# Kernel optimization log

Measured on AMD Instinct MI355X. Metric: run time of the kernel, lower is better.

The kernel has to match this reference:

```python
import jax, jax.numpy as jnp
import numpy as np

N, M, F, NBR = 100000, 12, 64, 64
EPS = 1e-5


def setup_inputs() -> dict:
    key = jax.random.key(0)
    ks = jax.random.split(key, 6)
    atom_in_fea = jax.random.normal(ks[0], (N, F), dtype=jnp.float32)
    nbr_fea = jax.random.normal(ks[1], (N, M, NBR), dtype=jnp.float32)
    bond_weights = jax.random.uniform(ks[2], (N, M), dtype=jnp.float32)
    nbr_fea_idx = jax.random.randint(ks[3], (N, M), 0, N)
    W = jax.random.normal(ks[4], (2 * F, 2 * F + NBR), dtype=jnp.float32) * 0.05
    b = jnp.zeros((2 * F,), dtype=jnp.float32)
    gamma1 = jnp.ones((2 * F,), dtype=jnp.float32)
    beta1 = jnp.zeros((2 * F,), dtype=jnp.float32)
    gamma2 = jnp.ones((F,), dtype=jnp.float32)
    beta2 = jnp.zeros((F,), dtype=jnp.float32)
    return dict(atom_in_fea=atom_in_fea, nbr_fea=nbr_fea, bond_weights=bond_weights,
                nbr_fea_idx=nbr_fea_idx, W=W, b=b, gamma1=gamma1, beta1=beta1,
                gamma2=gamma2, beta2=beta2)


def _batchnorm(x, gamma, beta):
    # training-mode BN over axis 0 with biased variance (torch BatchNorm1d)
    mean = x.mean(axis=0)
    var = ((x - mean) ** 2).mean(axis=0)
    return (x - mean) * jax.lax.rsqrt(var + EPS) * gamma + beta


def reference(atom_in_fea, nbr_fea, bond_weights, nbr_fea_idx, W, b,
              gamma1, beta1, gamma2, beta2):
    n, m = nbr_fea_idx.shape
    f = atom_in_fea.shape[1]
    atom_nbr_fea = atom_in_fea[nbr_fea_idx]                      # (N, M, F) gather
    self_fea = jnp.broadcast_to(atom_in_fea[:, None, :], (n, m, f))
    total = jnp.concatenate([self_fea, atom_nbr_fea, nbr_fea], axis=2)  # (N, M, 2F+NBR)
    gated = jnp.einsum('nmk,ok->nmo', total, W) + b              # (N, M, 2F)
    gated = _batchnorm(gated.reshape(-1, 2 * f), gamma1, beta1).reshape(n, m, 2 * f)
    nbr_filter = jax.nn.sigmoid(gated[..., :f]) * bond_weights[..., None]
    nbr_core = jax.nn.softplus(gated[..., f:]) * bond_weights[..., None]
    nbr_sumed = jnp.sum(nbr_filter * nbr_core, axis=1)           # (N, F)
    nbr_sumed = _batchnorm(nbr_sumed, gamma2, beta2)
    return jax.nn.softplus(atom_in_fea + nbr_sumed)
```

## Files before the change

### kernel.cpp

```cpp
#include <hip/hip_runtime.h>
#include <hip/hip_bf16.h>

typedef unsigned short ushort_t;
typedef __attribute__((ext_vector_type(8))) short bf16x8;
typedef __attribute__((ext_vector_type(4))) float f32x4;

#define NATOM 100000
#define NM    12
#define FD    64
#define KD    192
#define OD    128
#define NGRP  6250
#define ROWS1 1200000.0f
#define EPSBN 1e-5f


__device__ __forceinline__ float bf2f(ushort_t u) {
    unsigned int x = ((unsigned int)u) << 16;
    float f; __builtin_memcpy(&f, &x, 4); return f;
}
__device__ __forceinline__ ushort_t f2b(float f) {
    unsigned int x; __builtin_memcpy(&x, &f, 4);
    x += 0x7FFFu + ((x >> 16) & 1u);
    return (ushort_t)(x >> 16);
}

template<int DT>
__device__ __forceinline__ float ld1(const void* p, long i) {
    if constexpr (DT == 1) return bf2f(((const ushort_t*)p)[i]);
    else                   return ((const float*)p)[i];
}
template<int DT>
__device__ __forceinline__ void st1(void* p, long i, float v) {
    if constexpr (DT == 1) ((ushort_t*)p)[i] = f2b(v);
    else                   ((float*)p)[i] = v;
}
template<int DT>
__device__ __forceinline__ bf16x8 ld8(const void* p, long i) {
    if constexpr (DT == 1) {
        return *(const bf16x8*)((const ushort_t*)p + i);
    } else {
        const float4* f = (const float4*)((const float*)p + i);
        float4 a = f[0], b = f[1];
        bf16x8 r;
        r[0] = (short)f2b(a.x); r[1] = (short)f2b(a.y);
        r[2] = (short)f2b(a.z); r[3] = (short)f2b(a.w);
        r[4] = (short)f2b(b.x); r[5] = (short)f2b(b.y);
        r[6] = (short)f2b(b.z); r[7] = (short)f2b(b.w);
        return r;
    }
}

__global__ void k0_flag(const unsigned int* __restrict__ g1w, int* __restrict__ flag) {
    if (threadIdx.x == 0 && blockIdx.x == 0)
        *flag = (g1w[0] == 0x3F800000u) ? 0 : 1;
}

template<int DT>
__device__ __forceinline__ void stage_W(bf16x8* Wlds, const void* Wg, int tid) {
    for (int c = tid; c < 3072; c += 256) {
        int g = c >> 6, l = c & 63;
        int t = g / 6, s = g % 6;
        int row = t * 16 + (l & 15);
        int col = s * 32 + (l >> 4) * 8;
        Wlds[c] = ld8<DT>(Wg, row * KD + col);
    }
}

template<int DT>
__global__ __launch_bounds__(256) void k1_stats(
    const void* __restrict__ atomg, const void* __restrict__ nbrg,
    const int* __restrict__ idxg, const void* __restrict__ Wg,
    const int* __restrict__ flag, float* __restrict__ s1sum, float* __restrict__ s1sq)
{
    if (*flag != DT) return;
    __shared__ __align__(16) bf16x8 Wlds[3072];
    const int tid = threadIdx.x;
    const int w = tid >> 6, lane = tid & 63, la = lane & 15, q = lane >> 4;

    stage_W<DT>(Wlds, Wg, tid);
    __syncthreads();

    float sum[8], sq[8];
#pragma unroll
    for (int t = 0; t < 8; ++t) { sum[t] = 0.f; sq[t] = 0.f; }

    for (int grp = blockIdx.x; grp < NGRP; grp += gridDim.x) {
        const int n0 = grp << 4;
        const long selfo = (long)(n0 + la) * FD + q * 8;
        for (int it = 0; it < 3; ++it) {
            const int m = it * 4 + w;
            const int nb = idxg[(n0 + la) * NM + m];

            bf16x8 af[6];
            af[0] = ld8<DT>(atomg, selfo);
            af[1] = ld8<DT>(atomg, selfo + 32);
            af[2] = ld8<DT>(atomg, (long)nb * FD + q * 8);
            af[3] = ld8<DT>(atomg, (long)nb * FD + q * 8 + 32);
            af[4] = ld8<DT>(nbrg, ((long)(n0 + la) * NM + m) * FD + q * 8);
            af[5] = ld8<DT>(nbrg, ((long)(n0 + la) * NM + m) * FD + q * 8 + 32);

            f32x4 acc[8];
#pragma unroll
            for (int t = 0; t < 8; ++t) acc[t] = (f32x4){0.f, 0.f, 0.f, 0.f};
#pragma unroll
            for (int s = 0; s < 6; ++s) {
#pragma unroll
                for (int t = 0; t < 8; ++t) {
                    bf16x8 bfr = Wlds[(t * 6 + s) * 64 + lane];
                    acc[t] = __builtin_amdgcn_mfma_f32_16x16x32_bf16(af[s], bfr, acc[t], 0, 0, 0);
                }
            }
#pragma unroll
            for (int t = 0; t < 8; ++t)
#pragma unroll
                for (int r = 0; r < 4; ++r) {
                    float v = acc[t][r];
                    sum[t] += v; sq[t] += v * v;
                }
        }
    }

    const int rep = blockIdx.x & 7;
#pragma unroll
    for (int t = 0; t < 8; ++t) {
        float s = sum[t], z = sq[t];
        s += __shfl_xor(s, 16); s += __shfl_xor(s, 32);
        z += __shfl_xor(z, 16); z += __shfl_xor(z, 32);
        if (lane < 16) {
            atomicAdd(&s1sum[rep * OD + t * 16 + lane], s);
            atomicAdd(&s1sq [rep * OD + t * 16 + lane], z);
        }
    }
}

template<int DT>
__global__ __launch_bounds__(256) void k2_main(
    const void* __restrict__ atomg, const void* __restrict__ nbrg,
    const void* __restrict__ bwg, const int* __restrict__ idxg,
    const void* __restrict__ Wg,
    const void* __restrict__ g1p, const void* __restrict__ b1p,
    const float* __restrict__ s1sum, const float* __restrict__ s1sq,
    const int* __restrict__ flag,
    void* __restrict__ nsum, float* __restrict__ s2sum, float* __restrict__ s2sq)
{
    if (*flag != DT) return;
    __shared__ __align__(16) bf16x8 Wlds[3072];
    __shared__ float pred[4][16][64];
    const int tid = threadIdx.x;
    const int w = tid >> 6, lane = tid & 63, la = lane & 15, q = lane >> 4;

    stage_W<DT>(Wlds, Wg, tid);

    float scale[8], shift[8];
#pragma unroll
    for (int t = 0; t < 8; ++t) {
        int o = t * 16 + la;
        float sm = 0.f, sv = 0.f;
#pragma unroll
        for (int r = 0; r < 8; ++r) { sm += s1sum[r * OD + o]; sv += s1sq[r * OD + o]; }
        float mean = sm / ROWS1;
        float var  = sv / ROWS1 - mean * mean;
        float inv  = 1.0f / sqrtf(var + EPSBN);
        float ga   = ld1<DT>(g1p, o) * inv;
        scale[t] = ga;
        shift[t] = ld1<DT>(b1p, o) - mean * ga;
    }
    __syncthreads();

    float bsum = 0.f, bsq = 0.f;

    for (int grp = blockIdx.x; grp < NGRP; grp += gridDim.x) {
        const int n0 = grp << 4;
        const long selfo = (long)(n0 + la) * FD + q * 8;
        float psum[4][4];
#pragma unroll
        for (int t = 0; t < 4; ++t)
#pragma unroll
            for (int r = 0; r < 4; ++r) psum[t][r] = 0.f;

        for (int it = 0; it < 3; ++it) {
            const int m = it * 4 + w;
            const int nb = idxg[(n0 + la) * NM + m];

            bf16x8 af[6];
            af[0] = ld8<DT>(atomg, selfo);
            af[1] = ld8<DT>(atomg, selfo + 32);
            af[2] = ld8<DT>(atomg, (long)nb * FD + q * 8);
            af[3] = ld8<DT>(atomg, (long)nb * FD + q * 8 + 32);
            af[4] = ld8<DT>(nbrg, ((long)(n0 + la) * NM + m) * FD + q * 8);
            af[5] = ld8<DT>(nbrg, ((long)(n0 + la) * NM + m) * FD + q * 8 + 32);

            f32x4 acc[8];
#pragma unroll
            for (int t = 0; t < 8; ++t) acc[t] = (f32x4){0.f, 0.f, 0.f, 0.f};
#pragma unroll
            for (int s = 0; s < 6; ++s) {
#pragma unroll
                for (int t = 0; t < 8; ++t) {
                    bf16x8 bfr = Wlds[(t * 6 + s) * 64 + lane];
                    acc[t] = __builtin_amdgcn_mfma_f32_16x16x32_bf16(af[s], bfr, acc[t], 0, 0, 0);
                }
            }
#pragma unroll
            for (int r = 0; r < 4; ++r) {
                float bwv = ld1<DT>(bwg, (long)(n0 + q * 4 + r) * NM + m);
                float b2 = bwv * bwv;
#pragma unroll
                for (int t = 0; t < 4; ++t) {
                    float y1 = acc[t][r]     * scale[t]     + shift[t];
                    float y2 = acc[t + 4][r] * scale[t + 4] + shift[t + 4];
                    float sg = 1.0f / (1.0f + __expf(-y1));
                    float ax = fabsf(y2);
                    float sp = fmaxf(y2, 0.0f) + __logf(1.0f + __expf(-ax));
                    psum[t][r] += sg * sp * b2;
                }
            }
        }

#pragma unroll
        for (int t = 0; t < 4; ++t)
#pragma unroll
            for (int r = 0; r < 4; ++r)
                pred[w][q * 4 + r][t * 16 + la] = psum[t][r];
        __syncthreads();
        for (int e = tid; e < 1024; e += 256) {
            int a = e >> 6, c = e & 63;
            float v = pred[0][a][c] + pred[1][a][c] + pred[2][a][c] + pred[3][a][c];
            float vr;
            if constexpr (DT == 1) {
                ushort_t h = f2b(v);
                ((ushort_t*)nsum)[(long)(n0 + a) * FD + c] = h;
                vr = bf2f(h);
            } else {
                ((float*)nsum)[(long)(n0 + a) * FD + c] = v;
                vr = v;
            }
            bsum += vr; bsq += vr * vr;
        }
        __syncthreads();
    }

    const int rep = blockIdx.x & 7;
    atomicAdd(&s2sum[rep * FD + (tid & 63)], bsum);
    atomicAdd(&s2sq [rep * FD + (tid & 63)], bsq);
}

template<int DT>
__global__ __launch_bounds__(256) void k3_final(
    const void* __restrict__ atomg, void* __restrict__ nsum_out,
    const float* __restrict__ s2sum, const float* __restrict__ s2sq,
    const void* __restrict__ g2p, const void* __restrict__ b2p,
    const int* __restrict__ flag)
{
    if (*flag != DT) return;
    const int tid = blockIdx.x * 256 + threadIdx.x;
    const int c = tid & 63;
    float sm = 0.f, sv = 0.f;
#pragma unroll
    for (int r = 0; r < 8; ++r) { sm += s2sum[r * FD + c]; sv += s2sq[r * FD + c]; }
    float mean = sm / 100000.0f;
    float var  = sv / 100000.0f - mean * mean;
    float inv  = 1.0f / sqrtf(var + EPSBN);
    float ga   = ld1<DT>(g2p, c) * inv;
    float sh   = ld1<DT>(b2p, c) - mean * ga;
    float v = ld1<DT>(nsum_out, tid) * ga + sh + ld1<DT>(atomg, tid);
    float ax = fabsf(v);
    float sp = fmaxf(v, 0.0f) + __logf(1.0f + __expf(-ax));
    st1<DT>(nsum_out, tid, sp);
}

extern "C" void kernel_launch(void* const* d_in, const int* in_sizes, int n_in,
                              void* d_out, int out_size, void* d_ws, size_t ws_size,
                              hipStream_t stream) {
    const void* atomg = d_in[0];
    const void* nbrg  = d_in[1];
    const void* bwg   = d_in[2];
    const int*  idxg  = (const int*)d_in[3];
    const void* Wg    = d_in[4];
    const void* g1p   = d_in[6];
    const void* b1p   = d_in[7];
    const void* g2p   = d_in[8];
    const void* b2p   = d_in[9];

    float* wsf   = (float*)d_ws;
    float* s1sum = wsf;
    float* s1sq  = wsf + 1024;
    float* s2sum = wsf + 2048;
    float* s2sq  = wsf + 2560;
    int*   flag  = (int*)(wsf + 4000);

    hipMemsetAsync(d_ws, 0, 16384, stream);

    k0_flag<<<1, 64, 0, stream>>>((const unsigned int*)g1p, flag);

    k1_stats<0><<<768, 256, 0, stream>>>(atomg, nbrg, idxg, Wg, flag, s1sum, s1sq);
    k1_stats<1><<<768, 256, 0, stream>>>(atomg, nbrg, idxg, Wg, flag, s1sum, s1sq);

    k2_main<0><<<512, 256, 0, stream>>>(atomg, nbrg, bwg, idxg, Wg, g1p, b1p,
                                        s1sum, s1sq, flag, d_out, s2sum, s2sq);
    k2_main<1><<<512, 256, 0, stream>>>(atomg, nbrg, bwg, idxg, Wg, g1p, b1p,
                                        s1sum, s1sq, flag, d_out, s2sum, s2sq);

    k3_final<0><<<(NATOM * FD) / 256, 256, 0, stream>>>(atomg, d_out, s2sum, s2sq,
                                                        g2p, b2p, flag);
    k3_final<1><<<(NATOM * FD) / 256, 256, 0, stream>>>(atomg, d_out, s2sum, s2sq,
                                                        g2p, b2p, flag);
}
```

Baseline: 974.1 us.

## Remap k2 rows so each wave owns whole atoms; reduce via shuffles, prefetch loads

In k2, the 16 MFMA rows of each wave now hold 4 atoms × 4 neighbor slots instead of 16 atoms × 1 slot. This lets the per-atom neighbor sum be finished with cross-lane shuffles rather than an LDS buffer and two block barriers per group. Both k1 and k2 hoist the self-feature and index loads out of the neighbor loop; k1 also issues all gathers for a group before its MFMAs so the loads overlap. Launch bounds now request 3 blocks per CU and the k2 grid grows to 768, which trades register headroom for occupancy.

```diff
diff --git a/kernel.cpp b/kernel.cpp
--- a/kernel.cpp
+++ b/kernel.cpp
@@ -68,7 +68,7 @@
 }
 
 template<int DT>
-__global__ __launch_bounds__(256) void k1_stats(
+__global__ __launch_bounds__(256, 3) void k1_stats(
     const void* __restrict__ atomg, const void* __restrict__ nbrg,
     const int* __restrict__ idxg, const void* __restrict__ Wg,
     const int* __restrict__ flag, float* __restrict__ s1sum, float* __restrict__ s1sq)
@@ -88,21 +88,31 @@
     for (int grp = blockIdx.x; grp < NGRP; grp += gridDim.x) {
         const int n0 = grp << 4;
         const long selfo = (long)(n0 + la) * FD + q * 8;
+
+        const int ib = (n0 + la) * NM + w;
+        int nbv[3] = { idxg[ib], idxg[ib + 4], idxg[ib + 8] };
+
+        bf16x8 s0 = ld8<DT>(atomg, selfo);
+        bf16x8 s1 = ld8<DT>(atomg, selfo + 32);
+
+        bf16x8 a2[3], a3[3], a4[3], a5[3];
+#pragma unroll
         for (int it = 0; it < 3; ++it) {
             const int m = it * 4 + w;
-            const int nb = idxg[(n0 + la) * NM + m];
-
-            bf16x8 af[6];
-            af[0] = ld8<DT>(atomg, selfo);
-            af[1] = ld8<DT>(atomg, selfo + 32);
-            af[2] = ld8<DT>(atomg, (long)nb * FD + q * 8);
-            af[3] = ld8<DT>(atomg, (long)nb * FD + q * 8 + 32);
-            af[4] = ld8<DT>(nbrg, ((long)(n0 + la) * NM + m) * FD + q * 8);
-            af[5] = ld8<DT>(nbrg, ((long)(n0 + la) * NM + m) * FD + q * 8 + 32);
-
+            const long go = (long)nbv[it] * FD + q * 8;
+            a2[it] = ld8<DT>(atomg, go);
+            a3[it] = ld8<DT>(atomg, go + 32);
+            const long no = ((long)(n0 + la) * NM + m) * FD + q * 8;
+            a4[it] = ld8<DT>(nbrg, no);
+            a5[it] = ld8<DT>(nbrg, no + 32);
+        }
+
+#pragma unroll
+        for (int it = 0; it < 3; ++it) {
             f32x4 acc[8];
 #pragma unroll
             for (int t = 0; t < 8; ++t) acc[t] = (f32x4){0.f, 0.f, 0.f, 0.f};
+            bf16x8 af[6] = { s0, s1, a2[it], a3[it], a4[it], a5[it] };
 #pragma unroll
             for (int s = 0; s < 6; ++s) {
 #pragma unroll
@@ -135,7 +145,7 @@
 }
 
 template<int DT>
-__global__ __launch_bounds__(256) void k2_main(
+__global__ __launch_bounds__(256, 3) void k2_main(
     const void* __restrict__ atomg, const void* __restrict__ nbrg,
     const void* __restrict__ bwg, const int* __restrict__ idxg,
     const void* __restrict__ Wg,
@@ -146,9 +156,10 @@
 {
     if (*flag != DT) return;
     __shared__ __align__(16) bf16x8 Wlds[3072];
-    __shared__ float pred[4][16][64];
     const int tid = threadIdx.x;
     const int w = tid >> 6, lane = tid & 63, la = lane & 15, q = lane >> 4;
+    const int atom_l = la & 3;
+    const int msub   = la >> 2;
 
     stage_W<DT>(Wlds, Wg, tid);
 
@@ -168,32 +179,47 @@
     }
     __syncthreads();
 
-    float bsum = 0.f, bsq = 0.f;
+    float bs[4] = {0.f, 0.f, 0.f, 0.f};
+    float bq[4] = {0.f, 0.f, 0.f, 0.f};
 
     for (int grp = blockIdx.x; grp < NGRP; grp += gridDim.x) {
         const int n0 = grp << 4;
-        const long selfo = (long)(n0 + la) * FD + q * 8;
+        const int a0 = n0 + w * 4;
+        const int arow = a0 + atom_l;
+
+        const int ib = arow * NM + msub;
+        int nbv[3] = { idxg[ib], idxg[ib + 4], idxg[ib + 8] };
+
+        const long so = (long)arow * FD + q * 8;
+        bf16x8 s0 = ld8<DT>(atomg, so);
+        bf16x8 s1 = ld8<DT>(atomg, so + 32);
+
         float psum[4][4];
 #pragma unroll
         for (int t = 0; t < 4; ++t)
 #pragma unroll
             for (int r = 0; r < 4; ++r) psum[t][r] = 0.f;
 
+#pragma unroll
         for (int it = 0; it < 3; ++it) {
-            const int m = it * 4 + w;
-            const int nb = idxg[(n0 + la) * NM + m];
-
-            bf16x8 af[6];
-            af[0] = ld8<DT>(atomg, selfo);
-            af[1] = ld8<DT>(atomg, selfo + 32);
-            af[2] = ld8<DT>(atomg, (long)nb * FD + q * 8);
-            af[3] = ld8<DT>(atomg, (long)nb * FD + q * 8 + 32);
-            af[4] = ld8<DT>(nbrg, ((long)(n0 + la) * NM + m) * FD + q * 8);
-            af[5] = ld8<DT>(nbrg, ((long)(n0 + la) * NM + m) * FD + q * 8 + 32);
+            const long go = (long)nbv[it] * FD + q * 8;
+            bf16x8 a2 = ld8<DT>(atomg, go);
+            bf16x8 a3 = ld8<DT>(atomg, go + 32);
+            const long no = ((long)arow * NM + (msub + 4 * it)) * FD + q * 8;
+            bf16x8 a4 = ld8<DT>(nbrg, no);
+            bf16x8 a5 = ld8<DT>(nbrg, no + 32);
+
+            float bw2[4];
+#pragma unroll
+            for (int r = 0; r < 4; ++r) {
+                float bv = ld1<DT>(bwg, (long)(a0 + r) * NM + q + 4 * it);
+                bw2[r] = bv * bv;
+            }
 
             f32x4 acc[8];
 #pragma unroll
             for (int t = 0; t < 8; ++t) acc[t] = (f32x4){0.f, 0.f, 0.f, 0.f};
+            bf16x8 af[6] = { s0, s1, a2, a3, a4, a5 };
 #pragma unroll
             for (int s = 0; s < 6; ++s) {
 #pragma unroll
@@ -204,8 +230,6 @@
             }
 #pragma unroll
             for (int r = 0; r < 4; ++r) {
-                float bwv = ld1<DT>(bwg, (long)(n0 + q * 4 + r) * NM + m);
-                float b2 = bwv * bwv;
 #pragma unroll
                 for (int t = 0; t < 4; ++t) {
                     float y1 = acc[t][r]     * scale[t]     + shift[t];
@@ -213,37 +237,46 @@
                     float sg = 1.0f / (1.0f + __expf(-y1));
                     float ax = fabsf(y2);
                     float sp = fmaxf(y2, 0.0f) + __logf(1.0f + __expf(-ax));
-                    psum[t][r] += sg * sp * b2;
+                    psum[t][r] += sg * sp * bw2[r];
                 }
             }
         }
 
 #pragma unroll
-        for (int t = 0; t < 4; ++t)
-#pragma unroll
-            for (int r = 0; r < 4; ++r)
-                pred[w][q * 4 + r][t * 16 + la] = psum[t][r];
-        __syncthreads();
-        for (int e = tid; e < 1024; e += 256) {
-            int a = e >> 6, c = e & 63;
-            float v = pred[0][a][c] + pred[1][a][c] + pred[2][a][c] + pred[3][a][c];
+        for (int t = 0; t < 4; ++t) {
+#pragma unroll
+            for (int r = 0; r < 4; ++r) {
+                float v = psum[t][r];
+                v += __shfl_xor(v, 16);
+                v += __shfl_xor(v, 32);
+                psum[t][r] = v;
+            }
+            float v = (q == 0) ? psum[t][0] : (q == 1) ? psum[t][1]
+                    : (q == 2) ? psum[t][2] : psum[t][3];
             float vr;
             if constexpr (DT == 1) {
                 ushort_t h = f2b(v);
-                ((ushort_t*)nsum)[(long)(n0 + a) * FD + c] = h;
+                ((ushort_t*)nsum)[(long)(a0 + q) * FD + t * 16 + la] = h;
                 vr = bf2f(h);
             } else {
-                ((float*)nsum)[(long)(n0 + a) * FD + c] = v;
+                ((float*)nsum)[(long)(a0 + q) * FD + t * 16 + la] = v;
                 vr = v;
             }
-            bsum += vr; bsq += vr * vr;
-        }
-        __syncthreads();
+            bs[t] += vr; bq[t] += vr * vr;
+        }
     }
 
     const int rep = blockIdx.x & 7;
-    atomicAdd(&s2sum[rep * FD + (tid & 63)], bsum);
-    atomicAdd(&s2sq [rep * FD + (tid & 63)], bsq);
+#pragma unroll
+    for (int t = 0; t < 4; ++t) {
+        float s = bs[t], z = bq[t];
+        s += __shfl_xor(s, 16); s += __shfl_xor(s, 32);
+        z += __shfl_xor(z, 16); z += __shfl_xor(z, 32);
+        if (q == 0) {
+            atomicAdd(&s2sum[rep * FD + t * 16 + la], s);
+            atomicAdd(&s2sq [rep * FD + t * 16 + la], z);
+        }
+    }
 }
 
 template<int DT>
@@ -297,9 +330,9 @@
     k1_stats<0><<<768, 256, 0, stream>>>(atomg, nbrg, idxg, Wg, flag, s1sum, s1sq);
     k1_stats<1><<<768, 256, 0, stream>>>(atomg, nbrg, idxg, Wg, flag, s1sum, s1sq);
 
-    k2_main<0><<<512, 256, 0, stream>>>(atomg, nbrg, bwg, idxg, Wg, g1p, b1p,
+    k2_main<0><<<768, 256, 0, stream>>>(atomg, nbrg, bwg, idxg, Wg, g1p, b1p,
                                         s1sum, s1sq, flag, d_out, s2sum, s2sq);
-    k2_main<1><<<512, 256, 0, stream>>>(atomg, nbrg, bwg, idxg, Wg, g1p, b1p,
+    k2_main<1><<<768, 256, 0, stream>>>(atomg, nbrg, bwg, idxg, Wg, g1p, b1p,
                                         s1sum, s1sq, flag, d_out, s2sum, s2sq);
 
     k3_final<0><<<(NATOM * FD) / 256, 256, 0, stream>>>(atomg, d_out, s2sum, s2sq,
```

Result: slower. 1.489 ms (+52.8%).
